# Kernel optimization log

Hardware: AMD Instinct MI355X
Metric: run time of the kernel (lower is better)

The kernel has to match this reference:

```python
import jax, jax.numpy as jnp
import numpy as np

B, S, V, D, H, NL, FF, MAXD, OUTLEN, NC = 8, 1024, 64, 512, 8, 6, 2048, 64, 8, 10
HD = D // H


def _layernorm(x, g, b, eps=1e-5):
    m = jnp.mean(x, axis=-1, keepdims=True)
    v = jnp.var(x, axis=-1, keepdims=True)
    return (x - m) * jax.lax.rsqrt(v + eps) * g + b


def setup_inputs() -> dict:
    key = jax.random.key(0)
    ks = jax.random.split(key, 24)
    s = 0.02
    inp = {
        'src': jax.random.randint(ks[0], (B, S), 0, V, dtype=jnp.int32),
        'src_pad_mask': jnp.zeros((B, S), dtype=bool),
        'embed': jax.random.normal(ks[1], (V, D), jnp.float32) * s,
        'cls_token': jnp.zeros((D,), jnp.float32),
        'qkv_w': jax.random.normal(ks[2], (NL, 3 * D, D), jnp.float32) * s,
        'qkv_b': jnp.zeros((NL, 3 * D), jnp.float32),
        'out_w': jax.random.normal(ks[3], (NL, D, D), jnp.float32) * s,
        'out_b': jnp.zeros((NL, D), jnp.float32),
        'rel_emb': jax.random.normal(ks[4], (NL, 2 * MAXD + 1, H), jnp.float32) * s,
        'ln1_g': jnp.ones((NL, D), jnp.float32),
        'ln1_b': jnp.zeros((NL, D), jnp.float32),
        'w1': jax.random.normal(ks[5], (NL, FF, D), jnp.float32) * s,
        'b1': jnp.zeros((NL, FF), jnp.float32),
        'w2': jax.random.normal(ks[6], (NL, D, FF), jnp.float32) * s,
        'b2': jnp.zeros((NL, D), jnp.float32),
        'ln2_g': jnp.ones((NL, D), jnp.float32),
        'ln2_b': jnp.zeros((NL, D), jnp.float32),
        'norm_g': jnp.ones((D,), jnp.float32),
        'norm_b': jnp.zeros((D,), jnp.float32),
        'cls_w': jax.random.normal(ks[7], (OUTLEN * NC, D), jnp.float32) * s,
        'cls_b': jnp.zeros((OUTLEN * NC,), jnp.float32),
    }
    return inp


def _forward(src, src_pad_mask, embed, cls_token, qkv_w, qkv_b, out_w, out_b,
             rel_emb, ln1_g, ln1_b, w1, b1, w2, b2, ln2_g, ln2_b,
             norm_g, norm_b, cls_w, cls_b):
    b = src.shape[0]
    x = embed[src]                                         # [B,S,D]
    cls = jnp.broadcast_to(cls_token, (b, 1, D))
    x = jnp.concatenate([cls, x], axis=1)                  # [B,L,D], L=S+1
    L = x.shape[1]
    full_mask = jnp.concatenate([jnp.zeros((b, 1), bool), src_pad_mask], axis=1)

    # relative position indices, shared across layers
    rel = jnp.arange(L)[None, :] - jnp.arange(L)[:, None]  # [L,L]
    maxd = (rel_emb.shape[1] - 1) // 2
    rel = jnp.clip(rel, -maxd, maxd) + maxd
    scale = HD ** -0.5
    neg = jnp.asarray(-1e9, x.dtype)

    def layer(x, p):
        (qw, qb, ow, ob, re, g1, be1, W1, B1, W2, B2, g2, be2) = p
        qkv = jnp.einsum('bld,ed->ble', x, qw) + qb        # [B,L,3D]
        q, k, v = jnp.split(qkv, 3, axis=-1)
        q = q.reshape(b, L, H, HD)
        k = k.reshape(b, L, H, HD)
        v = v.reshape(b, L, H, HD)
        scores = jnp.einsum('bqhd,bkhd->bhqk', q, k) * scale
        bias = re[rel]                                     # [L,L,H]
        scores = scores + jnp.transpose(bias, (2, 0, 1))[None]
        scores = jnp.where(full_mask[:, None, None, :], neg, scores)
        attn = jax.nn.softmax(scores, axis=-1)
        o = jnp.einsum('bhqk,bkhd->bqhd', attn, v).reshape(b, L, D)
        o = jnp.einsum('bld,ed->ble', o, ow) + ob
        x2 = _layernorm(x + o, g1, be1)
        h = jax.nn.gelu(jnp.einsum('bld,fd->blf', x2, W1) + B1, approximate=False)
        ff = jnp.einsum('blf,df->bld', h, W2) + B2
        x3 = _layernorm(x2 + ff, g2, be2)
        return x3, None

    xs = (qkv_w, qkv_b, out_w, out_b, rel_emb, ln1_g, ln1_b,
          w1, b1, w2, b2, ln2_g, ln2_b)
    x, _ = jax.lax.scan(layer, x, xs)
    x = _layernorm(x, norm_g, norm_b)
    cls_repr = x[:, 0, :]
    logits = jnp.einsum('bd,od->bo', cls_repr, cls_w) + cls_b
    return logits.reshape(b, OUTLEN, NC)


def reference(src, src_pad_mask, embed, cls_token, qkv_w, qkv_b, out_w, out_b,
              rel_emb, ln1_g, ln1_b, w1, b1, w2, b2, ln2_g, ln2_b,
              norm_g, norm_b, cls_w, cls_b):
    return _forward(src, src_pad_mask, embed, cls_token, qkv_w, qkv_b, out_w,
                    out_b, rel_emb, ln1_g, ln1_b, w1, b1, w2, b2, ln2_g,
                    ln2_b, norm_g, norm_b, cls_w, cls_b)
```

## Files before the change

### kernel.cpp

```cpp
#include <hip/hip_runtime.h>
#include <hip/hip_bf16.h>
#include <stdint.h>

#define B 8
#define S 1024
#define L 1025
#define D 512
#define H 8
#define HD 64
#define NL 6
#define FF 2048
#define MAXD 64
#define OUTLEN 8
#define NC 10

#define MP 8320

typedef __bf16 bf16;
typedef __bf16 bf16x8 __attribute__((ext_vector_type(8)));
typedef __bf16 bf16x4 __attribute__((ext_vector_type(4)));
typedef __bf16 bf16x2 __attribute__((ext_vector_type(2)));
typedef float f32x4 __attribute__((ext_vector_type(4)));

__device__ __forceinline__ float fexp2(float x) { return __builtin_amdgcn_exp2f(x); }

#define LGKM_BARRIER() asm volatile("s_waitcnt lgkmcnt(0)\ns_barrier" ::: "memory")

__device__ __forceinline__ void gld16(const void* g, void* l) {
    __builtin_amdgcn_global_load_lds(
        (const __attribute__((address_space(1))) unsigned int*)g,
        (__attribute__((address_space(3))) unsigned int*)l,
        16, 0, 0);
}

__device__ __forceinline__ float fast_gelu(float v) {
    float x = v * 0.70710678118654752f;
    float ax = fabsf(x);
    float t = 1.f / fmaf(0.3275911f, ax, 1.f);
    float poly = t * (0.254829592f + t * (-0.284496736f + t * (1.421413741f +
                 t * (-1.453152027f + t * 1.061405429f))));
    float e = fexp2(-ax * ax * 1.4426950408889634f);
    float erfv = 1.f - poly * e;
    erfv = copysignf(erfv, x);
    return 0.5f * v * (1.f + erfv);
}

__global__ __launch_bounds__(256) void cvt_k(const float* __restrict__ in,
                                             bf16* __restrict__ out, int n4)
{
    int i = blockIdx.x * 256 + threadIdx.x;
    if (i >= n4) return;
    float4 v = reinterpret_cast<const float4*>(in)[i];
    bf16x4 o;
    o[0] = (bf16)v.x; o[1] = (bf16)v.y; o[2] = (bf16)v.z; o[3] = (bf16)v.w;
    reinterpret_cast<bf16x4*>(out)[i] = o;
}

__global__ void embed_k(const int* __restrict__ src, const float* __restrict__ emb,
                        const float* __restrict__ cls, bf16* __restrict__ xb)
{
    long i = (long)blockIdx.x * blockDim.x + threadIdx.x;
    if (i >= (long)B * L * D) return;
    int d = (int)(i % D);
    long bl = i / D;
    int l = (int)(bl % L);
    int b = (int)(bl / L);
    float v = (l == 0) ? cls[d] : emb[(long)src[b * S + (l - 1)] * D + d];
    xb[i] = (bf16)v;
}

template<int ACT, int OBF, int BIAS, int RT>
__global__ __launch_bounds__(256) void mgemm(const bf16* __restrict__ A,
                                             const bf16* __restrict__ W,
                                             const float* __restrict__ bias,
                                             float* __restrict__ Cf,
                                             bf16* __restrict__ Cb,
                                             int N, int K, int LDA)
{
    __shared__ bf16 Asl[2][RT * 32];
    __shared__ bf16 Bsl[2][128 * 32];
    int tid = threadIdx.x;
    int m0 = blockIdx.y * RT;
    int n0 = blockIdx.x * 128;
    int lane = tid & 63;
    int w = tid >> 6;
    int wbase = tid & ~63;
    int kb = (lane >> 4) * 8;
    int rsel = lane & 15;
    constexpr int FJ = (RT == 128) ? 4 : 2;
    constexpr int CW = (RT == 128) ? 64 : 32;
    int wr, wc;
    if constexpr (RT == 128) { wr = w >> 1; wc = w & 1; }
    else                     { wr = 0;      wc = w;     }
    f32x4 acc[4][FJ] = {};

    auto stage = [&](int buf, int k0) {
        if constexpr (RT == 128) {
#pragma unroll
            for (int r = 0; r < 2; r++) {
                int s = r * 256 + tid;
                int sb = r * 256 + wbase;
                gld16(A + (size_t)(m0 + (s >> 2)) * LDA + k0 + (s & 3) * 8, &Asl[buf][(size_t)sb * 8]);
                gld16(W + (size_t)(n0 + (s >> 2)) * LDA + k0 + (s & 3) * 8, &Bsl[buf][(size_t)sb * 8]);
            }
        } else {
            gld16(A + (size_t)(m0 + (tid >> 2)) * LDA + k0 + (tid & 3) * 8, &Asl[buf][(size_t)wbase * 8]);
#pragma unroll
            for (int r = 0; r < 2; r++) {
                int s = r * 256 + tid;
                int sb = r * 256 + wbase;
                gld16(W + (size_t)(n0 + (s >> 2)) * LDA + k0 + (s & 3) * 8, &Bsl[buf][(size_t)sb * 8]);
            }
        }
    };

    stage(0, 0);
    __syncthreads();

    for (int k0 = 0; k0 < K; k0 += 32) {
        int cur = (k0 >> 5) & 1;
        if (k0 + 32 < K) stage(cur ^ 1, k0 + 32);
        bf16x8 af[4], bfr[FJ];
#pragma unroll
        for (int fi = 0; fi < 4; fi++)
            af[fi] = *reinterpret_cast<const bf16x8*>(&Asl[cur][(wr * 64 + fi * 16 + rsel) * 32 + kb]);
#pragma unroll
        for (int fj = 0; fj < FJ; fj++)
            bfr[fj] = *reinterpret_cast<const bf16x8*>(&Bsl[cur][(wc * CW + fj * 16 + rsel) * 32 + kb]);
#pragma unroll
        for (int fi = 0; fi < 4; fi++)
#pragma unroll
            for (int fj = 0; fj < FJ; fj++)
                acc[fi][fj] = __builtin_amdgcn_mfma_f32_16x16x32_bf16(af[fi], bfr[fj], acc[fi][fj], 0, 0, 0);
        __syncthreads();
    }
    int rowb = (lane >> 4) * 4;
    int colb = lane & 15;
#pragma unroll
    for (int fi = 0; fi < 4; fi++) {
#pragma unroll
        for (int fj = 0; fj < FJ; fj++) {
            int col = n0 + wc * CW + fj * 16 + colb;
            float bsv = BIAS ? bias[col] : 0.f;
#pragma unroll
            for (int i = 0; i < 4; i++) {
                int row = m0 + wr * 64 + fi * 16 + rowb + i;
                float v = acc[fi][fj][i] + bsv;
                if (ACT) v = fast_gelu(v);
                if (OBF) Cb[(size_t)row * N + col] = (bf16)v;
                else     Cf[(size_t)row * N + col] = v;
            }
        }
    }
}

__global__ __launch_bounds__(256) void fattn_k(const bf16* __restrict__ qkv,
                                               const float* __restrict__ rel_emb_l,
                                               const unsigned char* __restrict__ pad,
                                               bf16* __restrict__ op0,
                                               bf16* __restrict__ op1,
                                               float2* __restrict__ mlout)
{
    constexpr int PIT = 72;
    __shared__ bf16 Vt[3][64 * PIT];
    __shared__ bf16 Psh[4][2][16 * PIT];
    __shared__ float bias2s[2 * MAXD + 1];
    __shared__ float colm[2][64];

    const int bh = blockIdx.x;
    const int qt = blockIdx.y;
    const int z = blockIdx.z;
    const int tbeg = z ? 9 : 0;
    const int tend = z ? 17 : 9;
    bf16* opart = z ? op1 : op0;
    const int h = bh & 7, b = bh >> 3;
    const int q0 = qt * 128;
    const int tid = threadIdx.x;
    const int lane = tid & 63;
    const int w = tid >> 6;
    const int ln15 = lane & 15, g4 = lane >> 4;
    const int kb8 = g4 * 8;
    constexpr float LOG2E = 1.4426950408889634f;
    constexpr float C2 = 0.125f * LOG2E;

    const char* base = (const char*)qkv + (size_t)(b * L) * 3072 + (size_t)h * (HD * 2);

    for (int i = tid; i < 2 * MAXD + 1; i += 256) bias2s[i] = rel_emb_l[i * H + h] * LOG2E;
    if (tid < 64) {
        int gk0 = tbeg * 64 + tid;
        int pi = (gk0 > 0 && gk0 <= 1024) ? gk0 - 1 : 0;
        colm[tbeg & 1][tid] = (gk0 > 1024 || (gk0 > 0 && pad[(size_t)b * S + pi])) ? -1e9f : 0.f;
    }

    int qrow[2];
    bf16x8 qa[2][2];
#pragma unroll
    for (int qq = 0; qq < 2; qq++) {
        qrow[qq] = q0 + qq * 64 + w * 16 + ln15;
        qa[qq][0] = *(const bf16x8*)(base + (size_t)qrow[qq] * 3072 + g4 * 16);
        qa[qq][1] = *(const bf16x8*)(base + (size_t)qrow[qq] * 3072 + 64 + g4 * 16);
    }

    const int vr = tid >> 3;
    const int vd0 = (tid & 7) * 8;
    const int vsw = ((vd0 >> 3) & 7) << 3;

    {
        int kv0 = tbeg * 64;
        bf16x8 a = *(const bf16x8*)(base + (size_t)(kv0 + vr) * 3072 + 2048 + vd0 * 2);
        bf16x8 c = *(const bf16x8*)(base + (size_t)(kv0 + vr + 32) * 3072 + 2048 + vd0 * 2);
#pragma unroll
        for (int j = 0; j < 8; j++) {
            Vt[0][(vd0 + j) * PIT + (vr ^ vsw)] = a[j];
            Vt[0][(vd0 + j) * PIT + ((vr + 32) ^ vsw)] = c[j];
        }
    }
    bf16x8 kr[4][2];
#pragma unroll
    for (int fj = 0; fj < 4; fj++) {
        const char* rp = base + (size_t)(tbeg * 64 + fj * 16 + ln15) * 3072 + 1024 + g4 * 16;
        kr[fj][0] = *(const bf16x8*)(rp);
        kr[fj][1] = *(const bf16x8*)(rp + 64);
    }
    LGKM_BARRIER();

    f32x4 oacc[2][4] = {};
    float m_prev[2] = {-1e30f, -1e30f};
    float l_sum[2] = {0.f, 0.f};

    int cur3 = 0;
    for (int t = tbeg; t < tend; t++) {
        const int k0 = t * 64;
        const int k0n = (k0 + 64 > 1024) ? 1024 : (k0 + 64);
        const int curM = t & 1;
        int nxt3 = cur3 + 1; if (nxt3 == 3) nxt3 = 0;

        bf16x8 vA = *(const bf16x8*)(base + (size_t)(k0n + vr) * 3072 + 2048 + vd0 * 2);
        bf16x8 vB = *(const bf16x8*)(base + (size_t)(k0n + vr + 32) * 3072 + 2048 + vd0 * 2);

        f32x4 sacc[2][4] = {};
#pragma unroll
        for (int qq = 0; qq < 2; qq++)
#pragma unroll
            for (int fj = 0; fj < 4; fj++) {
                sacc[qq][fj] = __builtin_amdgcn_mfma_f32_16x16x32_bf16(kr[fj][0], qa[qq][0], sacc[qq][fj], 0, 0, 0);
                sacc[qq][fj] = __builtin_amdgcn_mfma_f32_16x16x32_bf16(kr[fj][1], qa[qq][1], sacc[qq][fj], 0, 0, 0);
            }
#pragma unroll
        for (int fj = 0; fj < 4; fj++) {
            const char* rp = base + (size_t)(k0n + fj * 16 + ln15) * 3072 + 1024 + g4 * 16;
            kr[fj][0] = *(const bf16x8*)(rp);
            kr[fj][1] = *(const bf16x8*)(rp + 64);
        }

        f32x4 cm[4];
#pragma unroll
        for (int fj = 0; fj < 4; fj++)
            cm[fj] = *(const f32x4*)&colm[curM][fj * 16 + g4 * 4];

#pragma unroll
        for (int qq = 0; qq < 2; qq++) {
            float sv[4][4];
            const int relbw = k0 - q0 - qq * 64 - w * 16;
            if (relbw >= MAXD + 15 || relbw <= -MAXD - 63) {
                const float bu = bias2s[relbw > 0 ? 2 * MAXD : 0];
#pragma unroll
                for (int fj = 0; fj < 4; fj++)
#pragma unroll
                    for (int i = 0; i < 4; i++)
                        sv[fj][i] = fmaf(sacc[qq][fj][i], C2, bu + cm[fj][i]);
            } else {
                const int relb = k0 - qrow[qq];
#pragma unroll
                for (int fj = 0; fj < 4; fj++)
#pragma unroll
                    for (int i = 0; i < 4; i++) {
                        int rel = relb + fj * 16 + g4 * 4 + i;
                        rel = rel < -MAXD ? -MAXD : (rel > MAXD ? MAXD : rel);
                        sv[fj][i] = fmaf(sacc[qq][fj][i], C2, bias2s[rel + MAXD] + cm[fj][i]);
                    }
            }

            float mx = sv[0][0];
#pragma unroll
            for (int fj = 0; fj < 4; fj++)
#pragma unroll
                for (int i = 0; i < 4; i++) mx = fmaxf(mx, sv[fj][i]);
            mx = fmaxf(mx, __shfl_xor(mx, 16));
            mx = fmaxf(mx, __shfl_xor(mx, 32));
            const float mnew = fmaxf(m_prev[qq], mx);
            const float corr = fexp2(m_prev[qq] - mnew);
            float rsum = 0.f;
            float pb[4][4];
#pragma unroll
            for (int fj = 0; fj < 4; fj++)
#pragma unroll
                for (int i = 0; i < 4; i++) {
                    float p = fexp2(sv[fj][i] - mnew);
                    pb[fj][i] = p;
                    rsum += p;
                }
            rsum += __shfl_xor(rsum, 16);
            rsum += __shfl_xor(rsum, 32);
            l_sum[qq] = l_sum[qq] * corr + rsum;
            m_prev[qq] = mnew;
#pragma unroll
            for (int fd = 0; fd < 4; fd++) oacc[qq][fd] *= corr;

#pragma unroll
            for (int fj = 0; fj < 4; fj++) {
                union { bf16 hh[4]; unsigned long long u; } pk;
                pk.hh[0] = (bf16)pb[fj][0]; pk.hh[1] = (bf16)pb[fj][1];
                pk.hh[2] = (bf16)pb[fj][2]; pk.hh[3] = (bf16)pb[fj][3];
                *(unsigned long long*)&Psh[w][qq][ln15 * PIT + fj * 16 + g4 * 4] = pk.u;
            }
        }

#pragma unroll
        for (int j = 0; j < 8; j++) {
            Vt[nxt3][(vd0 + j) * PIT + (vr ^ vsw)] = vA[j];
            Vt[nxt3][(vd0 + j) * PIT + ((vr + 32) ^ vsw)] = vB[j];
        }
        if (tid < 64) {
            int gk = k0 + 64 + tid;
            int pi = (gk <= 1024) ? gk - 1 : 0;
            colm[curM ^ 1][tid] = (gk > 1024 || pad[(size_t)b * S + pi]) ? -1e9f : 0.f;
        }

        LGKM_BARRIER();

        bf16x8 pa[2][2];
#pragma unroll
        for (int qq = 0; qq < 2; qq++) {
            pa[qq][0] = *(const bf16x8*)&Psh[w][qq][ln15 * PIT + kb8];
            pa[qq][1] = *(const bf16x8*)&Psh[w][qq][ln15 * PIT + 32 + kb8];
        }
#pragma unroll
        for (int fd = 0; fd < 4; fd++) {
            const int d = fd * 16 + ln15;
            const int vx = ((d >> 3) & 7) << 3;
            bf16x8 af0 = *(const bf16x8*)&Vt[cur3][d * PIT + (kb8 ^ vx)];
            bf16x8 af1 = *(const bf16x8*)&Vt[cur3][d * PIT + ((32 + kb8) ^ vx)];
            oacc[0][fd] = __builtin_amdgcn_mfma_f32_16x16x32_bf16(af0, pa[0][0], oacc[0][fd], 0, 0, 0);
            oacc[0][fd] = __builtin_amdgcn_mfma_f32_16x16x32_bf16(af1, pa[0][1], oacc[0][fd], 0, 0, 0);
            oacc[1][fd] = __builtin_amdgcn_mfma_f32_16x16x32_bf16(af0, pa[1][0], oacc[1][fd], 0, 0, 0);
            oacc[1][fd] = __builtin_amdgcn_mfma_f32_16x16x32_bf16(af1, pa[1][1], oacc[1][fd], 0, 0, 0);
        }
        cur3 = nxt3;
    }

#pragma unroll
    for (int qq = 0; qq < 2; qq++) {
        if (qrow[qq] < L) {
            const float inv = 1.f / l_sum[qq];
            bf16* op = opart + (size_t)(b * L + qrow[qq]) * D + h * HD + g4 * 4;
#pragma unroll
            for (int fd = 0; fd < 4; fd++) {
                bf16x4 r;
#pragma unroll
                for (int i = 0; i < 4; i++) r[i] = (bf16)(oacc[qq][fd][i] * inv);
                *(bf16x4*)(op + fd * 16) = r;
            }
            if (g4 == 0)
                mlout[(size_t)(z * 64 + b * 8 + h) * 1025 + qrow[qq]] =
                    make_float2(m_prev[qq], l_sum[qq]);
        }
    }
}

__global__ __launch_bounds__(256) void comb_k(const bf16* __restrict__ op0,
                                              const bf16* __restrict__ op1,
                                              const float2* __restrict__ ml,
                                              bf16* __restrict__ ob)
{
    int row = blockIdx.x;
    int b = row / L, q = row - b * L;
    int tid = threadIdx.x;
    int d = tid & 63;
    int h0 = tid >> 6;
#pragma unroll
    for (int hh = 0; hh < 2; hh++) {
        int h = h0 + hh * 4;
        float2 a = ml[(size_t)(b * 8 + h) * 1025 + q];
        float2 c = ml[(size_t)(64 + b * 8 + h) * 1025 + q];
        float m = fmaxf(a.x, c.x);
        float s1 = a.y * fexp2(a.x - m);
        float s2 = c.y * fexp2(c.x - m);
        float inv = 1.f / (s1 + s2);
        size_t idx = (size_t)row * D + h * HD + d;
        float o = (s1 * (float)op0[idx] + s2 * (float)op1[idx]) * inv;
        ob[idx] = (bf16)o;
    }
}

__global__ __launch_bounds__(256) void add_ln_k(const bf16* __restrict__ xin,
                                                const bf16* __restrict__ rin,
                                                const float* __restrict__ g,
                                                const float* __restrict__ bb,
                                                bf16* __restrict__ outb)
{
    int row = blockIdx.x;
    __shared__ float red[8];
    int tid = threadIdx.x;
    bf16x2 a = reinterpret_cast<const bf16x2*>(xin + (size_t)row * D)[tid];
    bf16x2 r = reinterpret_cast<const bf16x2*>(rin + (size_t)row * D)[tid];
    float v0 = (float)a[0] + (float)r[0];
    float v1 = (float)a[1] + (float)r[1];
    float s = v0 + v1;
    for (int off = 32; off; off >>= 1) s += __shfl_down(s, off, 64);
    int lane = tid & 63, wid = tid >> 6;
    if (lane == 0) red[wid] = s;
    __syncthreads();
    if (tid == 0) red[0] = red[0] + red[1] + red[2] + red[3];
    __syncthreads();
    float mean = red[0] * (1.f / D);
    float d0 = v0 - mean, d1 = v1 - mean;
    float sq = d0 * d0 + d1 * d1;
    for (int off = 32; off; off >>= 1) sq += __shfl_down(sq, off, 64);
    if (lane == 0) red[4 + wid] = sq;
    __syncthreads();
    if (tid == 0) red[4] = red[4] + red[5] + red[6] + red[7];
    __syncthreads();
    float rs = rsqrtf(red[4] * (1.f / D) + 1e-5f);
    float r0 = d0 * rs * g[2 * tid] + bb[2 * tid];
    float r1 = d1 * rs * g[2 * tid + 1] + bb[2 * tid + 1];
    bf16x2 o;
    o[0] = (bf16)r0; o[1] = (bf16)r1;
    reinterpret_cast<bf16x2*>(outb + (size_t)row * D)[tid] = o;
}

__global__ __launch_bounds__(256) void cls_k(const bf16* __restrict__ x,
                                             const float* __restrict__ ng,
                                             const float* __restrict__ nb,
                                             const float* __restrict__ cw,
                                             const float* __restrict__ cb,
                                             float* __restrict__ out)
{
    int b = blockIdx.x;
    __shared__ float xn[D];
    __shared__ float red[8];
    int tid = threadIdx.x;
    const bf16* xp = x + (size_t)(b * L) * D;
    float v0 = (float)xp[tid], v1 = (float)xp[tid + 256];
    float s = v0 + v1;
    for (int off = 32; off; off >>= 1) s += __shfl_down(s, off, 64);
    int lane = tid & 63, wid = tid >> 6;
    if (lane == 0) red[wid] = s;
    __syncthreads();
    if (tid == 0) red[0] = red[0] + red[1] + red[2] + red[3];
    __syncthreads();
    float mean = red[0] * (1.f / D);
    float d0 = v0 - mean, d1 = v1 - mean;
    float sq = d0 * d0 + d1 * d1;
    for (int off = 32; off; off >>= 1) sq += __shfl_down(sq, off, 64);
    if (lane == 0) red[4 + wid] = sq;
    __syncthreads();
    if (tid == 0) red[4] = red[4] + red[5] + red[6] + red[7];
    __syncthreads();
    float rs = rsqrtf(red[4] * (1.f / D) + 1e-5f);
    xn[tid] = d0 * rs * ng[tid] + nb[tid];
    xn[tid + 256] = d1 * rs * ng[tid + 256] + nb[tid + 256];
    __syncthreads();
    for (int o = tid; o < OUTLEN * NC; o += 256) {
        float acc = cb[o];
        const float* wp = cw + (size_t)o * D;
        for (int d = 0; d < D; d++) acc += xn[d] * wp[d];
        out[b * OUTLEN * NC + o] = acc;
    }
}

extern "C" void kernel_launch(void* const* d_in, const int* in_sizes, int n_in,
                              void* d_out, int out_size, void* d_ws, size_t ws_size,
                              hipStream_t stream) {
    const int* src = (const int*)d_in[0];
    const unsigned char* pad = (const unsigned char*)d_in[1];
    const float* emb = (const float*)d_in[2];
    const float* cls_token = (const float*)d_in[3];
    const float* qkv_w = (const float*)d_in[4];
    const float* qkv_b = (const float*)d_in[5];
    const float* out_w = (const float*)d_in[6];
    const float* out_b = (const float*)d_in[7];
    const float* rel_emb = (const float*)d_in[8];
    const float* ln1_g = (const float*)d_in[9];
    const float* ln1_b = (const float*)d_in[10];
    const float* w1 = (const float*)d_in[11];
    const float* b1 = (const float*)d_in[12];
    const float* w2 = (const float*)d_in[13];
    const float* b2 = (const float*)d_in[14];
    const float* ln2_g = (const float*)d_in[15];
    const float* ln2_b = (const float*)d_in[16];
    const float* norm_g = (const float*)d_in[17];
    const float* norm_b = (const float*)d_in[18];
    const float* cls_w = (const float*)d_in[19];
    const float* cls_b = (const float*)d_in[20];
    float* out = (float*)d_out;

    char* ws = (char*)d_ws;
    size_t off = 0;
    bf16*  xb  = (bf16*) (ws + off); off += (size_t)MP * D * 2;
    bf16*  x2b = (bf16*) (ws + off); off += (size_t)MP * D * 2;
    char*  R   = ws + off;           off += (size_t)MP * 3 * D * 4;
    bf16*  qkvb = (bf16*)R;
    bf16*  hb  = (bf16*)R;
    bf16*  pb  = (bf16*)(R + (size_t)MP * FF * 2);
    float2* mlbuf = (float2*)(R + (size_t)MP * FF * 2 + (size_t)MP * D * 2);
    bf16*  obf = (bf16*) (ws + off); off += (size_t)MP * D * 2;

    const size_t WQ = (size_t)NL * 3 * D * D;
    const size_t WO = (size_t)NL * D * D;
    const size_t W1E = (size_t)NL * FF * D;
    const size_t W2E = (size_t)NL * D * FF;
    const size_t WALL = WQ + WO + W1E + W2E;
    bool all_w = (off + WALL * 2) <= ws_size;

    bf16 *wq_a = nullptr, *wo_a = nullptr, *w1_a = nullptr, *w2_a = nullptr, *wbuf = nullptr;
    if (all_w) {
        wq_a = (bf16*)(ws + off);
        wo_a = wq_a + WQ;
        w1_a = wo_a + WO;
        w2_a = w1_a + W1E;
        int n4;
        n4 = (int)(WQ / 4);  cvt_k<<<dim3((n4 + 255) / 256), 256, 0, stream>>>(qkv_w, wq_a, n4);
        n4 = (int)(WO / 4);  cvt_k<<<dim3((n4 + 255) / 256), 256, 0, stream>>>(out_w, wo_a, n4);
        n4 = (int)(W1E / 4); cvt_k<<<dim3((n4 + 255) / 256), 256, 0, stream>>>(w1, w1_a, n4);
        n4 = (int)(W2E / 4); cvt_k<<<dim3((n4 + 255) / 256), 256, 0, stream>>>(w2, w2_a, n4);
    } else {
        wbuf = (bf16*)(ws + off);
    }

    const int M = B * L;
    {
        long total = (long)B * L * D;
        embed_k<<<dim3((unsigned)((total + 255) / 256)), 256, 0, stream>>>(src, emb, cls_token, xb);
    }
    for (int l = 0; l < NL; l++) {
        const float* qb  = qkv_b + (size_t)l * 3 * D;
        const float* obi = out_b + (size_t)l * D;
        const float* re  = rel_emb + (size_t)l * (2 * MAXD + 1) * H;
        const float* g1  = ln1_g + (size_t)l * D;
        const float* be1 = ln1_b + (size_t)l * D;
        const float* B1p = b1 + (size_t)l * FF;
        const float* B2p = b2 + (size_t)l * D;
        const float* g2  = ln2_g + (size_t)l * D;
        const float* be2 = ln2_b + (size_t)l * D;

        const bf16 *wqb, *wob, *w1b, *w2b;
        if (all_w) {
            wqb = wq_a + (size_t)l * 3 * D * D;
            wob = wo_a + (size_t)l * D * D;
            w1b = w1_a + (size_t)l * FF * D;
            w2b = w2_a + (size_t)l * D * FF;
        } else {
            bf16* wp_ = wbuf;
            wqb = wp_;            wp_ += 3 * D * D;
            wob = wp_;            wp_ += D * D;
            w1b = wp_;            wp_ += FF * D;
            w2b = wp_;
            int n4;
            n4 = 3 * D * D / 4; cvt_k<<<dim3((n4 + 255) / 256), 256, 0, stream>>>(qkv_w + (size_t)l * 3 * D * D, (bf16*)wqb, n4);
            n4 = D * D / 4;     cvt_k<<<dim3((n4 + 255) / 256), 256, 0, stream>>>(out_w + (size_t)l * D * D, (bf16*)wob, n4);
            n4 = FF * D / 4;    cvt_k<<<dim3((n4 + 255) / 256), 256, 0, stream>>>(w1 + (size_t)l * FF * D, (bf16*)w1b, n4);
            n4 = D * FF / 4;    cvt_k<<<dim3((n4 + 255) / 256), 256, 0, stream>>>(w2 + (size_t)l * D * FF, (bf16*)w2b, n4);
        }

        mgemm<0, 1, 1, 128><<<dim3(3 * D / 128, MP / 128), 256, 0, stream>>>(xb, wqb, qb, nullptr, qkvb, 3 * D, D, D);
        fattn_k<<<dim3(B * H, 9, 2), 256, 0, stream>>>(qkvb, re, pad, x2b, obf, mlbuf);
        comb_k<<<dim3(M), 256, 0, stream>>>(x2b, obf, mlbuf, obf);
        mgemm<0, 1, 1, 64><<<dim3(D / 128, MP / 64), 256, 0, stream>>>(obf, wob, obi, nullptr, pb, D, D, D);
        add_ln_k<<<dim3(M), 256, 0, stream>>>(xb, pb, g1, be1, x2b);
        mgemm<1, 1, 1, 128><<<dim3(FF / 128, MP / 128), 256, 0, stream>>>(x2b, w1b, B1p, nullptr, hb, FF, D, D);
        mgemm<0, 1, 1, 64><<<dim3(D / 128, MP / 64), 256, 0, stream>>>(hb, w2b, B2p, nullptr, pb, D, FF, FF);
        add_ln_k<<<dim3(M), 256, 0, stream>>>(x2b, pb, g2, be2, xb);
    }
    cls_k<<<dim3(B), 256, 0, stream>>>(xb, norm_g, norm_b, cls_w, cls_b, out);
}
```

Before: 1.418 ms.

## Add 256x256-tile 8-wave GEMM with staged prefetch for QKV and FFN1

Adds a new GEMM kernel with 512 threads, a 256x256 output tile and K-step 64. It double-buffers global-to-LDS loads in quarter stages interleaved with MFMA quads and raises wave priority around the MFMA blocks. The QKV and FFN-up projections use it in place of the 128x128 kernel, and the padded row count rises to a multiple of 256. The aim is more data reuse per tile and better overlap of loads with MFMA, at the cost of larger LDS use (128KB), fewer blocks (lower occupancy, possible tail effects on 304 CUs) and extra padded rows.

Measured after the change: 1.636 ms. 1.15x slower.

```diff
diff --git a/kernel.cpp b/kernel.cpp
--- a/kernel.cpp
+++ b/kernel.cpp
@@ -14,7 +14,7 @@
 #define OUTLEN 8
 #define NC 10
 
-#define MP 8320
+#define MP 8448
 
 typedef __bf16 bf16;
 typedef __bf16 bf16x8 __attribute__((ext_vector_type(8)));
@@ -67,6 +67,119 @@
     int b = (int)(bl / L);
     float v = (l == 0) ? cls[d] : emb[(long)src[b * S + (l - 1)] * D + d];
     xb[i] = (bf16)v;
+}
+
+template<int ACT>
+__global__ __launch_bounds__(512) void mgemm8(const bf16* __restrict__ A,
+                                              const bf16* __restrict__ W,
+                                              const float* __restrict__ bias,
+                                              bf16* __restrict__ Cb,
+                                              int N, int K)
+{
+    __shared__ bf16 Ab[2][256 * 64];
+    __shared__ bf16 Bb[2][256 * 64];
+    const int tid = threadIdx.x;
+    const int m0 = blockIdx.y * 256;
+    const int n0 = blockIdx.x * 256;
+    const int lane = tid & 63;
+    const int w = tid >> 6;
+    const int wm = w >> 2, wn = w & 3;
+    const int wbase = tid & ~63;
+    const int ln15 = lane & 15, g4 = lane >> 4;
+    const int NK = K >> 6;
+
+    f32x4 acc[8][4] = {};
+    bf16x8 afr[4][2], bfr[2][2];
+
+    auto stA = [&](int kt, int half) {
+        int buf = kt & 1, k0 = kt << 6;
+#pragma unroll
+        for (int gI = 0; gI < 2; gI++) {
+            int s = gI * 512 + tid, sb = gI * 512 + wbase;
+            gld16(A + (size_t)(m0 + half * 128 + (s >> 3)) * K + k0 + (s & 7) * 8,
+                  &Ab[buf][half * 8192 + sb * 8]);
+        }
+    };
+    auto stB = [&](int kt, int half) {
+        int buf = kt & 1, k0 = kt << 6;
+#pragma unroll
+        for (int gI = 0; gI < 2; gI++) {
+            int s = gI * 512 + tid, sb = gI * 512 + wbase;
+            gld16(W + (size_t)(n0 + half * 128 + (s >> 3)) * K + k0 + (s & 7) * 8,
+                  &Bb[buf][half * 8192 + sb * 8]);
+        }
+    };
+    auto ldA = [&](int buf, int qi) {
+        int rb = (wm * 128 + qi * 64 + ln15) * 64 + g4 * 8;
+#pragma unroll
+        for (int fi = 0; fi < 4; fi++) {
+            afr[fi][0] = *(const bf16x8*)&Ab[buf][rb + fi * 1024];
+            afr[fi][1] = *(const bf16x8*)&Ab[buf][rb + fi * 1024 + 32];
+        }
+    };
+    auto ldB = [&](int buf, int qj) {
+        int cb_ = (wn * 64 + qj * 32 + ln15) * 64 + g4 * 8;
+#pragma unroll
+        for (int fj = 0; fj < 2; fj++) {
+            bfr[fj][0] = *(const bf16x8*)&Bb[buf][cb_ + fj * 1024];
+            bfr[fj][1] = *(const bf16x8*)&Bb[buf][cb_ + fj * 1024 + 32];
+        }
+    };
+
+#define MFMA_QUAD(QI, QJ)                                                              \
+    __builtin_amdgcn_s_setprio(1);                                                     \
+    _Pragma("unroll")                                                                  \
+    for (int fi = 0; fi < 4; fi++) {                                                   \
+        _Pragma("unroll")                                                              \
+        for (int fj = 0; fj < 2; fj++) {                                               \
+            acc[(QI)*4+fi][(QJ)*2+fj] = __builtin_amdgcn_mfma_f32_16x16x32_bf16(       \
+                afr[fi][0], bfr[fj][0], acc[(QI)*4+fi][(QJ)*2+fj], 0, 0, 0);           \
+            acc[(QI)*4+fi][(QJ)*2+fj] = __builtin_amdgcn_mfma_f32_16x16x32_bf16(       \
+                afr[fi][1], bfr[fj][1], acc[(QI)*4+fi][(QJ)*2+fj], 0, 0, 0);           \
+        }                                                                              \
+    }                                                                                  \
+    __builtin_amdgcn_s_setprio(0);
+
+    stA(0, 0); stA(0, 1); stB(0, 0); stB(0, 1);
+    if (NK > 1) stA(1, 0);
+
+    for (int kt = 0; kt < NK; kt++) {
+        const int buf = kt & 1;
+        if (kt + 1 < NK) asm volatile("s_waitcnt vmcnt(2)\ns_barrier" ::: "memory");
+        else             asm volatile("s_waitcnt vmcnt(0)\ns_barrier" ::: "memory");
+        if (kt + 1 < NK) stA(kt + 1, 1);
+        ldA(buf, 0); ldB(buf, 0);
+        MFMA_QUAD(0, 0)
+        __builtin_amdgcn_s_barrier();
+        if (kt + 1 < NK) stB(kt + 1, 0);
+        ldB(buf, 1);
+        MFMA_QUAD(0, 1)
+        __builtin_amdgcn_s_barrier();
+        if (kt + 1 < NK) stB(kt + 1, 1);
+        ldA(buf, 1);
+        MFMA_QUAD(1, 1)
+        __builtin_amdgcn_s_barrier();
+        if (kt + 2 < NK) stA(kt + 2, 0);
+        ldB(buf, 0);
+        MFMA_QUAD(1, 0)
+    }
+
+#pragma unroll
+    for (int fi = 0; fi < 8; fi++) {
+#pragma unroll
+        for (int fj = 0; fj < 4; fj++) {
+            int col = n0 + wn * 64 + fj * 16 + ln15;
+            float bsv = bias[col];
+#pragma unroll
+            for (int i = 0; i < 4; i++) {
+                int row = m0 + wm * 128 + fi * 16 + g4 * 4 + i;
+                float v = acc[fi][fj][i] + bsv;
+                if (ACT) v = fast_gelu(v);
+                Cb[(size_t)row * N + col] = (bf16)v;
+            }
+        }
+    }
+#undef MFMA_QUAD
 }
 
 template<int ACT, int OBF, int BIAS, int RT>
@@ -563,12 +676,12 @@
             n4 = D * FF / 4;    cvt_k<<<dim3((n4 + 255) / 256), 256, 0, stream>>>(w2 + (size_t)l * D * FF, (bf16*)w2b, n4);
         }
 
-        mgemm<0, 1, 1, 128><<<dim3(3 * D / 128, MP / 128), 256, 0, stream>>>(xb, wqb, qb, nullptr, qkvb, 3 * D, D, D);
+        mgemm8<0><<<dim3(3 * D / 256, MP / 256), 512, 0, stream>>>(xb, wqb, qb, qkvb, 3 * D, D);
         fattn_k<<<dim3(B * H, 9, 2), 256, 0, stream>>>(qkvb, re, pad, x2b, obf, mlbuf);
         comb_k<<<dim3(M), 256, 0, stream>>>(x2b, obf, mlbuf, obf);
         mgemm<0, 1, 1, 64><<<dim3(D / 128, MP / 64), 256, 0, stream>>>(obf, wob, obi, nullptr, pb, D, D, D);
         add_ln_k<<<dim3(M), 256, 0, stream>>>(xb, pb, g1, be1, x2b);
-        mgemm<1, 1, 1, 128><<<dim3(FF / 128, MP / 128), 256, 0, stream>>>(x2b, w1b, B1p, nullptr, hb, FF, D, D);
+        mgemm8<1><<<dim3(FF / 256, MP / 256), 512, 0, stream>>>(x2b, w1b, B1p, hb, FF, D);
         mgemm<0, 1, 1, 64><<<dim3(D / 128, MP / 64), 256, 0, stream>>>(hb, w2b, B2p, nullptr, pb, D, FF, FF);
         add_ln_k<<<dim3(M), 256, 0, stream>>>(x2b, pb, g2, be2, xb);
     }
```
